# Performance work log

Hardware: AMD Instinct MI355X
Metric: run time of the kernel (lower is better)

## Reference

```python
import jax, jax.numpy as jnp
import numpy as np

N_NODES = 50000
N_EDGES = 800000
IN_DIM = 64
EDGE_DIM = 16
HID = 128
L = 3
G = 128  # number of graphs in the batch
EPS = 1e-5


def _glorot(key, shape):
    fan_in, fan_out = shape[0], shape[1]
    lim = float(np.sqrt(6.0 / (fan_in + fan_out)))
    return jax.random.uniform(key, shape, jnp.float32, -lim, lim)


def setup_inputs() -> dict:
    key = jax.random.key(0)
    ks = jax.random.split(key, 40)
    inp = {}
    inp["x"] = jax.random.uniform(ks[0], (N_NODES, IN_DIM), jnp.float32)
    inp["edge_index"] = jax.random.randint(ks[1], (2, N_EDGES), 0, N_NODES, jnp.int64)
    inp["edge_attr"] = jax.random.normal(ks[2], (N_EDGES, EDGE_DIM), jnp.float32)
    inp["batch"] = jnp.sort(jax.random.randint(ks[3], (N_NODES,), 0, G, jnp.int64))
    # ligand / protein input MLPs: Linear-ReLU-Linear-ReLU
    inp["lig_w1"] = _glorot(ks[4], (IN_DIM, HID)); inp["lig_b1"] = jnp.zeros((HID,), jnp.float32)
    inp["lig_w2"] = _glorot(ks[5], (HID, HID));    inp["lig_b2"] = jnp.zeros((HID,), jnp.float32)
    inp["prot_w1"] = _glorot(ks[6], (IN_DIM, HID)); inp["prot_b1"] = jnp.zeros((HID,), jnp.float32)
    inp["prot_w2"] = _glorot(ks[7], (HID, HID));    inp["prot_b2"] = jnp.zeros((HID,), jnp.float32)
    # per-layer GINEConv params (stacked over layers)
    inp["edge_w"] = jnp.stack([_glorot(ks[8 + i], (EDGE_DIM, HID)) for i in range(L)])
    inp["edge_b"] = jnp.zeros((L, HID), jnp.float32)
    inp["nn_w1"] = jnp.stack([_glorot(ks[12 + i], (HID, HID)) for i in range(L)])
    inp["nn_b1"] = jnp.zeros((L, HID), jnp.float32)
    inp["nn_w2"] = jnp.stack([_glorot(ks[16 + i], (HID, HID)) for i in range(L)])
    inp["nn_b2"] = jnp.zeros((L, HID), jnp.float32)
    # GraphNorm params: weight=1, bias=0, mean_scale=1
    inp["gn_w"] = jnp.ones((L, HID), jnp.float32)
    inp["gn_b"] = jnp.zeros((L, HID), jnp.float32)
    inp["gn_ms"] = jnp.ones((L, HID), jnp.float32)
    # output head: Linear-ReLU-Linear(1)
    inp["fc_w1"] = _glorot(ks[20], (HID, HID)); inp["fc_b1"] = jnp.zeros((HID,), jnp.float32)
    inp["fc_w2"] = _glorot(ks[21], (HID, 1));   inp["fc_b2"] = jnp.zeros((1,), jnp.float32)
    return inp


def reference(x, edge_index, edge_attr, batch,
              lig_w1, lig_b1, lig_w2, lig_b2,
              prot_w1, prot_b1, prot_w2, prot_b2,
              edge_w, edge_b, nn_w1, nn_b1, nn_w2, nn_b2,
              gn_w, gn_b, gn_ms,
              fc_w1, fc_b1, fc_w2, fc_b2):
    relu = lambda a: jnp.maximum(a, 0)
    src, dst = edge_index[0], edge_index[1]

    # input encoders, merged per node by protein flag (last feature column)
    is_prot = x[:, -1] > 0.5
    h_lig = relu(relu(x @ lig_w1 + lig_b1) @ lig_w2 + lig_b2)
    h_prot = relu(relu(x @ prot_w1 + prot_b1) @ prot_w2 + prot_b2)
    h = jnp.where(is_prot[:, None], h_prot, h_lig)

    # per-graph node counts for GraphNorm
    cnt = jax.ops.segment_sum(jnp.ones((x.shape[0],), jnp.float32), batch, num_segments=G)
    cnt = jnp.maximum(cnt, 1.0)[:, None]

    for l in range(L):
        # GINEConv (eps=0): out = nn(x + sum_{j->i} relu(x_j + lin(e_ji)))
        e = edge_attr @ edge_w[l] + edge_b[l]              # [E, HID]
        msg = relu(h[src] + e)                             # gather + add + relu
        aggr = jax.ops.segment_sum(msg, dst, num_segments=h.shape[0])
        h = aggr + h
        h = relu(h @ nn_w1[l] + nn_b1[l]) @ nn_w2[l] + nn_b2[l]
        # GraphNorm: per-graph mean/var with learnable mean_scale
        mean = jax.ops.segment_sum(h, batch, num_segments=G) / cnt
        hc = h - mean[batch] * gn_ms[l]
        var = jax.ops.segment_sum(hc * hc, batch, num_segments=G) / cnt
        h = gn_w[l] * hc * jax.lax.rsqrt(var[batch] + EPS) + gn_b[l]
        h = relu(h)  # (dropout=0.0 -> identity)

    g = jax.ops.segment_sum(h, batch, num_segments=G)      # global_add_pool
    out = relu(g @ fc_w1 + fc_b1) @ fc_w2 + fc_b2
    return out.reshape(-1)
```

## Files before the change

kernel.cpp:

```cpp
#include <hip/hip_runtime.h>

#define N_NODES 50000
#define N_EDGES 800000
#define IN_DIM  64
#define EDGE_DIM 16
#define HID     128
#define NLAYERS 3
#define NGRAPH  128
#define EPS     1e-5f

typedef __attribute__((ext_vector_type(8))) short bf8_t;
typedef __attribute__((ext_vector_type(4))) short bf4_t;
typedef __attribute__((ext_vector_type(4))) float f32x4;

__device__ __forceinline__ unsigned short f2bf(float x) {
    unsigned u = __float_as_uint(x);
    unsigned r = u + 0x7fffu + ((u >> 16) & 1u);
    return (unsigned short)(r >> 16);
}
__device__ __forceinline__ float bf2f(unsigned short v) {
    return __uint_as_float(((unsigned)v) << 16);
}

__global__ void k_init(int* __restrict__ row_cnt, float* __restrict__ pool,
                       float* __restrict__ gsum, float* __restrict__ gsq) {
    int i = blockIdx.x * blockDim.x + threadIdx.x;
    if (i < N_NODES) row_cnt[i] = 0;
    if (i < NGRAPH * HID) { pool[i] = 0.0f; gsum[i] = 0.0f; gsq[i] = 0.0f; }
}

__global__ __launch_bounds__(NGRAPH) void k_count(const int* __restrict__ batch,
                                                  float* __restrict__ cnt) {
    int g = threadIdx.x;
    int lo = 0, hi = N_NODES;
    while (lo < hi) { int mid = (lo + hi) >> 1; if (batch[mid] < g) lo = mid + 1; else hi = mid; }
    int a = lo;
    lo = 0; hi = N_NODES;
    while (lo < hi) { int mid = (lo + hi) >> 1; if (batch[mid] < g + 1) lo = mid + 1; else hi = mid; }
    cnt[g] = (float)(lo - a);
}

__global__ void k_wconv(const float* __restrict__ nw1, const float* __restrict__ nw2,
                        unsigned short* __restrict__ wt) {
    int idx = blockIdx.x * 256 + threadIdx.x;
    if (idx >= NLAYERS * 2 * HID * HID) return;
    int k = idx & 127;
    int n = (idx >> 7) & 127;
    int which = (idx >> 14) & 1;
    int l = idx >> 15;
    const float* w = (which == 0 ? nw1 : nw2) + l * HID * HID;
    wt[idx] = f2bf(w[k * HID + n]);
}

__global__ void k_wconv_enc(const float* __restrict__ lw1, const float* __restrict__ pw1,
                            const float* __restrict__ lw2, const float* __restrict__ pw2,
                            unsigned short* __restrict__ we) {
    int idx = blockIdx.x * 256 + threadIdx.x;
    if (idx >= 49152) return;
    float v;
    if (idx < 8192)       { int n = idx >> 6, k = idx & 63;            v = lw1[k * HID + n]; }
    else if (idx < 16384) { int r = idx - 8192;  int n = r >> 6, k = r & 63;  v = pw1[k * HID + n]; }
    else if (idx < 32768) { int r = idx - 16384; int n = r >> 7, k = r & 127; v = lw2[k * HID + n]; }
    else                  { int r = idx - 32768; int n = r >> 7, k = r & 127; v = pw2[k * HID + n]; }
    we[idx] = f2bf(v);
}

__global__ void k_wconv_e(const float* __restrict__ ew, const float* __restrict__ eb,
                          unsigned short* __restrict__ wte) {
    int idx = blockIdx.x * 256 + threadIdx.x;
    if (idx >= NLAYERS * 8 * 64 * 8) return;
    int j = idx & 7;
    int lane = (idx >> 3) & 63;
    int t = (idx >> 9) & 7;
    int l = idx >> 12;
    int k = (lane >> 4) * 8 + j;
    int feat = t * 16 + (lane & 15);
    float v = 0.0f;
    if (k < EDGE_DIM)       v = ew[l * EDGE_DIM * HID + k * HID + feat];
    else if (k == EDGE_DIM) v = eb[l * HID + feat];
    wte[idx] = f2bf(v);
}

__global__ void k_hist(const int* __restrict__ dsts, int* __restrict__ row_cnt) {
    int e = blockIdx.x * blockDim.x + threadIdx.x;
    if (e < N_EDGES) atomicAdd(&row_cnt[dsts[e]], 1);
}

__global__ __launch_bounds__(256) void k_scan1(const int* __restrict__ row_cnt,
                                               int* __restrict__ partial) {
    __shared__ int s[256];
    int t = threadIdx.x, b = blockIdx.x;
    int i0 = b * 512 + t;
    int v = 0;
    if (i0 < N_NODES) v += row_cnt[i0];
    if (i0 + 256 < N_NODES) v += row_cnt[i0 + 256];
    s[t] = v; __syncthreads();
    for (int off = 128; off > 0; off >>= 1) {
        if (t < off) s[t] += s[t + off];
        __syncthreads();
    }
    if (t == 0) partial[b] = s[0];
}

#define NCHUNK 98
__global__ __launch_bounds__(128) void k_scan2(int* __restrict__ partial) {
    __shared__ int s[128];
    int t = threadIdx.x;
    int v = (t < NCHUNK) ? partial[t] : 0;
    s[t] = v; __syncthreads();
    for (int off = 1; off < 128; off <<= 1) {
        int x = (t >= off) ? s[t - off] : 0;
        __syncthreads();
        s[t] += x;
        __syncthreads();
    }
    partial[t] = s[t] - v;
}

__global__ __launch_bounds__(512) void k_scan3(const int* __restrict__ row_cnt,
                                               const int* __restrict__ partial,
                                               int* __restrict__ row_start,
                                               int* __restrict__ row_fill) {
    __shared__ int s[512];
    int t = threadIdx.x, b = blockIdx.x;
    int i = b * 512 + t;
    int v = (i < N_NODES) ? row_cnt[i] : 0;
    s[t] = v; __syncthreads();
    for (int off = 1; off < 512; off <<= 1) {
        int x = (t >= off) ? s[t - off] : 0;
        __syncthreads();
        s[t] += x;
        __syncthreads();
    }
    int excl = s[t] - v + partial[b];
    if (i < N_NODES) { row_start[i] = excl; row_fill[i] = excl; }
}

__global__ void k_fill(const int* __restrict__ srcs, const int* __restrict__ dsts,
                       int* __restrict__ row_fill, int2* __restrict__ csr_se) {
    int e = blockIdx.x * blockDim.x + threadIdx.x;
    if (e < N_EDGES) {
        int p = atomicAdd(&row_fill[dsts[e]], 1);
        csr_se[p] = make_int2(srcs[e], e);
    }
}

__global__ __launch_bounds__(256) void k_reorder(const int2* __restrict__ csr_se,
                                                 const float* __restrict__ ea,
                                                 int* __restrict__ csr_src,
                                                 unsigned short* __restrict__ cea) {
    int p = blockIdx.x * blockDim.x + threadIdx.x;
    if (p < N_EDGES) {
        int2 se = csr_se[p];
        csr_src[p] = se.x;
        const float* s = ea + (size_t)se.y * EDGE_DIM;
        float4 a0 = *(const float4*)(s);
        float4 a1 = *(const float4*)(s + 4);
        float4 a2 = *(const float4*)(s + 8);
        float4 a3 = *(const float4*)(s + 12);
        bf8_t v0, v1;
        v0[0] = (short)f2bf(a0.x); v0[1] = (short)f2bf(a0.y);
        v0[2] = (short)f2bf(a0.z); v0[3] = (short)f2bf(a0.w);
        v0[4] = (short)f2bf(a1.x); v0[5] = (short)f2bf(a1.y);
        v0[6] = (short)f2bf(a1.z); v0[7] = (short)f2bf(a1.w);
        v1[0] = (short)f2bf(a2.x); v1[1] = (short)f2bf(a2.y);
        v1[2] = (short)f2bf(a2.z); v1[3] = (short)f2bf(a2.w);
        v1[4] = (short)f2bf(a3.x); v1[5] = (short)f2bf(a3.y);
        v1[6] = (short)f2bf(a3.z); v1[7] = (short)f2bf(a3.w);
        *(bf8_t*)(cea + (size_t)p * EDGE_DIM) = v0;
        *(bf8_t*)(cea + (size_t)p * EDGE_DIM + 8) = v1;
    }
}

#define HS 136
__global__ __launch_bounds__(256, 8) void k_encoder_mfma(
    const float* __restrict__ x,
    const unsigned short* __restrict__ we,
    const float* __restrict__ lb1, const float* __restrict__ lb2,
    const float* __restrict__ pb1, const float* __restrict__ pb2,
    unsigned short* __restrict__ Hbp) {
    __shared__ short h1s[4][16 * HS];
    int w = threadIdx.x >> 6, lane = threadIdx.x & 63;
    int m = lane & 15, quad = lane >> 4;
    int tile = w >> 1, role = w & 1;
    int nb = blockIdx.x * 32 + tile * 16;
    short* hl = h1s[w];
    int nclamp = nb + m; if (nclamp >= N_NODES) nclamp = N_NODES - 1;
    const float* xp = x + (size_t)nclamp * IN_DIM;
    const float* b1 = role ? pb1 : lb1;
    const float* b2 = role ? pb2 : lb2;
    const unsigned short* w1 = we + role * 8192;
    const unsigned short* w2 = we + 16384 + role * 16384;

    f32x4 a1[8];
    #pragma unroll
    for (int t = 0; t < 8; ++t) {
        float bv = b1[t * 16 + m];
        a1[t] = (f32x4){bv, bv, bv, bv};
    }
    #pragma unroll
    for (int s_ = 0; s_ < 2; ++s_) {
        int k0 = s_ * 32 + quad * 8;
        float4 a0 = *(const float4*)(xp + k0);
        float4 a1v = *(const float4*)(xp + k0 + 4);
        bf8_t af;
        af[0] = (short)f2bf(a0.x); af[1] = (short)f2bf(a0.y);
        af[2] = (short)f2bf(a0.z); af[3] = (short)f2bf(a0.w);
        af[4] = (short)f2bf(a1v.x); af[5] = (short)f2bf(a1v.y);
        af[6] = (short)f2bf(a1v.z); af[7] = (short)f2bf(a1v.w);
        #pragma unroll
        for (int t = 0; t < 8; ++t) {
            bf8_t bw = *(const bf8_t*)(w1 + (t * 16 + m) * 64 + k0);
            a1[t] = __builtin_amdgcn_mfma_f32_16x16x32_bf16(af, bw, a1[t], 0, 0, 0);
        }
    }
    #pragma unroll
    for (int t = 0; t < 8; ++t)
        #pragma unroll
        for (int r = 0; r < 4; ++r)
            hl[(quad * 4 + r) * HS + t * 16 + m] = (short)f2bf(fmaxf(a1[t][r], 0.0f));
    __syncthreads();
    f32x4 a2[8];
    #pragma unroll
    for (int t = 0; t < 8; ++t) {
        float bv = b2[t * 16 + m];
        a2[t] = (f32x4){bv, bv, bv, bv};
    }
    #pragma unroll
    for (int s_ = 0; s_ < 4; ++s_) {
        int k0 = s_ * 32 + quad * 8;
        bf8_t af = *(const bf8_t*)(hl + m * HS + k0);
        #pragma unroll
        for (int t = 0; t < 8; ++t) {
            bf8_t bw = *(const bf8_t*)(w2 + (t * 16 + m) * 128 + k0);
            a2[t] = __builtin_amdgcn_mfma_f32_16x16x32_bf16(af, bw, a2[t], 0, 0, 0);
        }
    }
    #pragma unroll
    for (int r = 0; r < 4; ++r) {
        int node = nb + quad * 4 + r;
        if (node < N_NODES) {
            bool prot = x[(size_t)node * IN_DIM + (IN_DIM - 1)] > 0.5f;
            if (prot == (role == 1)) {
                bf8_t o;
                #pragma unroll
                for (int t = 0; t < 8; ++t)
                    o[t] = (short)f2bf(fmaxf(a2[t][r], 0.0f));
                *(bf8_t*)(Hbp + (size_t)node * HID + m * 8) = o;
            }
        }
    }
}

__global__ __launch_bounds__(256, 8) void k_gather(
    const int* __restrict__ csr_src, const unsigned short* __restrict__ cea,
    const int* __restrict__ row_start, const int* __restrict__ row_end,
    const unsigned short* __restrict__ wte,
    const unsigned short* __restrict__ Hbp, unsigned short* __restrict__ Abp) {
    int w = threadIdx.x >> 6, lane = threadIdx.x & 63;
    int m = lane & 15, quad = lane >> 4;
    int n = blockIdx.x * 2 + (w >> 1);
    int half = w & 1;

    bf8_t bw[4];
    #pragma unroll
    for (int t = 0; t < 4; ++t)
        bw[t] = *(const bf8_t*)(wte + ((size_t)(half * 4 + t) * 64 + lane) * 8);

    float acc[4];
    #pragma unroll
    for (int t = 0; t < 4; ++t) acc[t] = 0.0f;

    int p  = __builtin_amdgcn_readfirstlane(row_start[n]);
    int pe = __builtin_amdgcn_readfirstlane(row_end[n]);

    const f32x4 zc = (f32x4){0.0f, 0.0f, 0.0f, 0.0f};

    for (; p + 16 <= pe; p += 16) {
        bf8_t af = (bf8_t){0, 0, 0, 0, 0, 0, 0, 0};
        if (quad < 2)
            af = *(const bf8_t*)(cea + (size_t)(p + m) * EDGE_DIM + quad * 8);
        else if (quad == 2)
            af[0] = (short)0x3F80;
        int sr[4];
        #pragma unroll
        for (int r = 0; r < 4; ++r) sr[r] = csr_src[p + quad * 4 + r];
        bf4_t hrow[4];
        #pragma unroll
        for (int r = 0; r < 4; ++r)
            hrow[r] = *(const bf4_t*)(Hbp + (size_t)sr[r] * HID + m * 8 + half * 4);
        f32x4 d[4];
        #pragma unroll
        for (int t = 0; t < 4; ++t)
            d[t] = __builtin_amdgcn_mfma_f32_16x16x32_bf16(af, bw[t], zc, 0, 0, 0);
        #pragma unroll
        for (int t = 0; t < 4; ++t)
            #pragma unroll
            for (int r = 0; r < 4; ++r)
                acc[t] += fmaxf(bf2f((unsigned short)hrow[r][t]) + d[t][r], 0.0f);
    }
    int rem = pe - p;
    if (rem > 0) {
        bf8_t af = (bf8_t){0, 0, 0, 0, 0, 0, 0, 0};
        if (quad < 2 && m < rem)
            af = *(const bf8_t*)(cea + (size_t)(p + m) * EDGE_DIM + quad * 8);
        else if (quad == 2)
            af[0] = (short)0x3F80;
        int sr[4];
        #pragma unroll
        for (int r = 0; r < 4; ++r) {
            int idx = p + quad * 4 + r; if (idx >= pe) idx = pe - 1;
            sr[r] = csr_src[idx];
        }
        bf4_t hrow[4];
        #pragma unroll
        for (int r = 0; r < 4; ++r)
            hrow[r] = *(const bf4_t*)(Hbp + (size_t)sr[r] * HID + m * 8 + half * 4);
        f32x4 d[4];
        #pragma unroll
        for (int t = 0; t < 4; ++t)
            d[t] = __builtin_amdgcn_mfma_f32_16x16x32_bf16(af, bw[t], zc, 0, 0, 0);
        #pragma unroll
        for (int t = 0; t < 4; ++t)
            #pragma unroll
            for (int r = 0; r < 4; ++r)
                if (quad * 4 + r < rem)
                    acc[t] += fmaxf(bf2f((unsigned short)hrow[r][t]) + d[t][r], 0.0f);
    }
    #pragma unroll
    for (int t = 0; t < 4; ++t) {
        acc[t] += __shfl_xor(acc[t], 16);
        acc[t] += __shfl_xor(acc[t], 32);
    }
    float asel = (quad == 0) ? acc[0] : (quad == 1) ? acc[1] : (quad == 2) ? acc[2] : acc[3];
    float self_ = bf2f(Hbp[(size_t)n * HID + m * 8 + half * 4 + quad]);
    Abp[(size_t)n * HID + (half * 4 + quad) * 16 + m] = f2bf(asel + self_);
}

#define MLP_NODES_PER_BLOCK 64
__global__ __launch_bounds__(256) void k_mlp_mfma(
    const unsigned short* __restrict__ Abp, const int* __restrict__ batch,
    const unsigned short* __restrict__ wt1, const unsigned short* __restrict__ wt2,
    const float* __restrict__ b1, const float* __restrict__ b2,
    unsigned short* __restrict__ Hb, float* __restrict__ gsum, float* __restrict__ gsq) {
    __shared__ short h1s[4 * 16 * HS];
    int w = threadIdx.x >> 6;
    int lane = threadIdx.x & 63;
    int m = lane & 15;
    int quad = lane >> 4;
    int nb = blockIdx.x * MLP_NODES_PER_BLOCK + w * 16;
    short* hw = h1s + w * 16 * HS;

    int nclamp = nb + m; if (nclamp >= N_NODES) nclamp = N_NODES - 1;
    const unsigned short* Ap = Abp + (size_t)nclamp * HID;
    f32x4 acc1[8];
    #pragma unroll
    for (int t = 0; t < 8; ++t) {
        float bv = b1[t * 16 + m];
        acc1[t] = (f32x4){bv, bv, bv, bv};
    }
    #pragma unroll
    for (int s_ = 0; s_ < 4; ++s_) {
        int k0 = s_ * 32 + quad * 8;
        bf8_t af = *(const bf8_t*)(Ap + k0);
        #pragma unroll
        for (int t = 0; t < 8; ++t) {
            bf8_t bf = *(const bf8_t*)(wt1 + (t * 16 + m) * HID + k0);
            acc1[t] = __builtin_amdgcn_mfma_f32_16x16x32_bf16(af, bf, acc1[t], 0, 0, 0);
        }
    }
    #pragma unroll
    for (int t = 0; t < 8; ++t)
        #pragma unroll
        for (int r = 0; r < 4; ++r) {
            float v = fmaxf(acc1[t][r], 0.0f);
            hw[(quad * 4 + r) * HS + t * 16 + m] = (short)f2bf(v);
        }
    __syncthreads();
    f32x4 acc2[8];
    #pragma unroll
    for (int t = 0; t < 8; ++t) {
        float bv = b2[t * 16 + m];
        acc2[t] = (f32x4){bv, bv, bv, bv};
    }
    #pragma unroll
    for (int s_ = 0; s_ < 4; ++s_) {
        int k0 = s_ * 32 + quad * 8;
        bf8_t af = *(const bf8_t*)(hw + m * HS + k0);
        #pragma unroll
        for (int t = 0; t < 8; ++t) {
            bf8_t bf = *(const bf8_t*)(wt2 + (t * 16 + m) * HID + k0);
            acc2[t] = __builtin_amdgcn_mfma_f32_16x16x32_bf16(af, bf, acc2[t], 0, 0, 0);
        }
    }
    #pragma unroll
    for (int t = 0; t < 8; ++t)
        #pragma unroll
        for (int r = 0; r < 4; ++r) {
            int node = nb + quad * 4 + r;
            if (node < N_NODES) Hb[(size_t)node * HID + t * 16 + m] = f2bf(acc2[t][r]);
        }
    int blast = nb + 15 < N_NODES ? batch[nb + 15] : -1;
    int g0 = batch[nb < N_NODES ? nb : N_NODES - 1];
    if (nb + 15 < N_NODES && g0 == blast) {
        #pragma unroll
        for (int t = 0; t < 8; ++t) {
            float s = 0.0f, q = 0.0f;
            #pragma unroll
            for (int r = 0; r < 4; ++r) { float v = acc2[t][r]; s += v; q += v * v; }
            s += __shfl_xor(s, 16); q += __shfl_xor(q, 16);
            s += __shfl_xor(s, 32); q += __shfl_xor(q, 32);
            if (quad == 0) {
                atomicAdd(&gsum[g0 * HID + t * 16 + m], s);
                atomicAdd(&gsq[g0 * HID + t * 16 + m], q);
            }
        }
    } else {
        #pragma unroll
        for (int t = 0; t < 8; ++t)
            #pragma unroll
            for (int r = 0; r < 4; ++r) {
                int node = nb + quad * 4 + r;
                if (node < N_NODES) {
                    int g = batch[node];
                    float v = acc2[t][r];
                    atomicAdd(&gsum[g * HID + t * 16 + m], v);
                    atomicAdd(&gsq[g * HID + t * 16 + m], v * v);
                }
            }
    }
}

__global__ __launch_bounds__(HID) void k_stats(
    float* __restrict__ gsum, float* __restrict__ gsq,
    const float* __restrict__ cnt,
    const float* __restrict__ gw, const float* __restrict__ gb,
    const float* __restrict__ gms,
    float* __restrict__ sc, float* __restrict__ of) {
    int g = blockIdx.x;
    int t = threadIdx.x;
    float c = fmaxf(cnt[g], 1.0f);
    float mean = gsum[g * HID + t] / c;
    float msq  = gsq[g * HID + t] / c;
    float ms = gms[t];
    float var = msq - mean * mean * ms * (2.0f - ms);
    var = fmaxf(var, 0.0f);
    float istd = rsqrtf(var + EPS);
    float s = gw[t] * istd;
    sc[g * HID + t] = s;
    of[g * HID + t] = gb[t] - s * mean * ms;
    gsum[g * HID + t] = 0.0f;
    gsq[g * HID + t]  = 0.0f;
}

#define NORM_N 8
__global__ __launch_bounds__(HID) void k_norm(
    const unsigned short* __restrict__ Hb, const int* __restrict__ batch,
    const float* __restrict__ sc, const float* __restrict__ of,
    unsigned short* __restrict__ Hbp, float* __restrict__ pool, int accumulate) {
    int n0 = blockIdx.x * NORM_N;
    int t = threadIdx.x;
    int m = t & 15, tt = t >> 4;
    int g0 = batch[n0], gN = batch[n0 + NORM_N - 1];
    if (g0 == gN) {
        float ssc = sc[g0 * HID + t], sof = of[g0 * HID + t];
        float ps = 0.0f;
        #pragma unroll
        for (int i = 0; i < NORM_N; ++i) {
            float v = fmaxf(bf2f(Hb[(size_t)(n0 + i) * HID + t]) * ssc + sof, 0.0f);
            Hbp[(size_t)(n0 + i) * HID + m * 8 + tt] = f2bf(v);
            ps += v;
        }
        if (accumulate) atomicAdd(&pool[g0 * HID + t], ps);
    } else {
        #pragma unroll
        for (int i = 0; i < NORM_N; ++i) {
            int g = batch[n0 + i];
            float v = fmaxf(bf2f(Hb[(size_t)(n0 + i) * HID + t]) * sc[g * HID + t] + of[g * HID + t], 0.0f);
            Hbp[(size_t)(n0 + i) * HID + m * 8 + tt] = f2bf(v);
            if (accumulate) atomicAdd(&pool[g * HID + t], v);
        }
    }
}

__global__ __launch_bounds__(HID) void k_head(
    const float* __restrict__ pool,
    const float* __restrict__ fw1, const float* __restrict__ fb1,
    const float* __restrict__ fw2, const float* __restrict__ fb2,
    float* __restrict__ out) {
    __shared__ float ps[HID];
    __shared__ float red[2];
    int g = blockIdx.x;
    int t = threadIdx.x;
    ps[t] = pool[g * HID + t];
    __syncthreads();
    float acc = fb1[t];
    #pragma unroll 4
    for (int k = 0; k < HID; ++k) acc = fmaf(ps[k], fw1[k * HID + t], acc);
    float p = fmaxf(acc, 0.0f) * fw2[t];
    #pragma unroll
    for (int off = 32; off > 0; off >>= 1) p += __shfl_down(p, off, 64);
    if ((t & 63) == 0) red[t >> 6] = p;
    __syncthreads();
    if (t == 0) out[g] = red[0] + red[1] + fb2[0];
}

extern "C" void kernel_launch(void* const* d_in, const int* in_sizes, int n_in,
                              void* d_out, int out_size, void* d_ws, size_t ws_size,
                              hipStream_t stream) {
    const float* x     = (const float*)d_in[0];
    const int*   ei    = (const int*)d_in[1];
    const float* ea    = (const float*)d_in[2];
    const int*   batch = (const int*)d_in[3];
    const float* lw1 = (const float*)d_in[4];
    const float* lb1 = (const float*)d_in[5];
    const float* lw2 = (const float*)d_in[6];
    const float* lb2 = (const float*)d_in[7];
    const float* pw1 = (const float*)d_in[8];
    const float* pb1 = (const float*)d_in[9];
    const float* pw2 = (const float*)d_in[10];
    const float* pb2 = (const float*)d_in[11];
    const float* ew  = (const float*)d_in[12];
    const float* eb  = (const float*)d_in[13];
    const float* nw1 = (const float*)d_in[14];
    const float* nb1 = (const float*)d_in[15];
    const float* nw2 = (const float*)d_in[16];
    const float* nb2 = (const float*)d_in[17];
    const float* gw  = (const float*)d_in[18];
    const float* gb  = (const float*)d_in[19];
    const float* gms = (const float*)d_in[20];
    const float* fw1 = (const float*)d_in[21];
    const float* fb1 = (const float*)d_in[22];
    const float* fw2 = (const float*)d_in[23];
    const float* fb2 = (const float*)d_in[24];
    float* out = (float*)d_out;

    float* ws   = (float*)d_ws;
    float* H    = ws;
    float* A    = H    + (size_t)N_NODES * HID;
    float* gsum = A    + (size_t)N_NODES * HID;
    float* gsq  = gsum + NGRAPH * HID;
    float* sc   = gsq  + NGRAPH * HID;
    float* of   = sc   + NGRAPH * HID;
    float* pool = of   + NGRAPH * HID;
    float* cnt  = pool + NGRAPH * HID;
    int* row_cnt   = (int*)(cnt + NGRAPH);
    int* row_start = row_cnt + N_NODES;
    int* row_fill  = row_start + N_NODES;
    int* partial   = row_fill + N_NODES;
    int* csr_src   = partial + 128;
    unsigned short* cea  = (unsigned short*)(csr_src + N_EDGES);
    unsigned short* wt   = cea + (size_t)N_EDGES * EDGE_DIM;
    unsigned short* wenc = wt + NLAYERS * 2 * HID * HID;
    unsigned short* wte  = wenc + 49152;
    unsigned short* Hbp  = wte + NLAYERS * 8 * 64 * 8;
    unsigned short* Hb   = (unsigned short*)H;
    unsigned short* Abp  = (unsigned short*)A;
    int2* csr_se = (int2*)(Abp + (size_t)N_NODES * HID);

    const int* srcs = ei;
    const int* dsts = ei + N_EDGES;

    k_init<<<(N_NODES + 255) / 256, 256, 0, stream>>>(row_cnt, pool, gsum, gsq);
    k_count<<<1, NGRAPH, 0, stream>>>(batch, cnt);
    k_wconv<<<(NLAYERS * 2 * HID * HID + 255) / 256, 256, 0, stream>>>(nw1, nw2, wt);
    k_wconv_enc<<<(49152 + 255) / 256, 256, 0, stream>>>(lw1, pw1, lw2, pw2, wenc);
    k_wconv_e<<<(NLAYERS * 8 * 64 * 8 + 255) / 256, 256, 0, stream>>>(ew, eb, wte);
    k_hist<<<(N_EDGES + 255) / 256, 256, 0, stream>>>(dsts, row_cnt);
    k_scan1<<<NCHUNK, 256, 0, stream>>>(row_cnt, partial);
    k_scan2<<<1, 128, 0, stream>>>(partial);
    k_scan3<<<NCHUNK, 512, 0, stream>>>(row_cnt, partial, row_start, row_fill);
    k_fill<<<(N_EDGES + 255) / 256, 256, 0, stream>>>(srcs, dsts, row_fill, csr_se);
    k_reorder<<<(N_EDGES + 255) / 256, 256, 0, stream>>>(csr_se, ea, csr_src, cea);

    k_encoder_mfma<<<(N_NODES + 31) / 32, 256, 0, stream>>>(
        x, wenc, lb1, lb2, pb1, pb2, Hbp);

    int mlp_blocks = (N_NODES + MLP_NODES_PER_BLOCK - 1) / MLP_NODES_PER_BLOCK;
    for (int l = 0; l < NLAYERS; ++l) {
        k_gather<<<N_NODES / 2, 256, 0, stream>>>(
            csr_src, cea, row_start, row_fill,
            wte + (size_t)l * 4096, Hbp, Abp);
        k_mlp_mfma<<<mlp_blocks, 256, 0, stream>>>(
            Abp, batch,
            wt + (size_t)l * 2 * HID * HID,
            wt + (size_t)l * 2 * HID * HID + HID * HID,
            nb1 + l * HID, nb2 + l * HID, Hb, gsum, gsq);
        k_stats<<<NGRAPH, HID, 0, stream>>>(gsum, gsq, cnt,
                                            gw + l * HID, gb + l * HID, gms + l * HID,
                                            sc, of);
        k_norm<<<N_NODES / NORM_N, HID, 0, stream>>>(
            Hb, batch, sc, of, Hbp, pool, (l == NLAYERS - 1) ? 1 : 0);
    }
    k_head<<<NGRAPH, HID, 0, stream>>>(pool, fw1, fb1, fw2, fb2, out);
}
```

Baseline: 674.1 us.

## Split MLP output features across wave pairs to cut accumulator registers

Each 16-node tile in the fused node MLP is now handled by two waves, each computing half of the 128 output features, and a block covers 32 nodes instead of 64. Per-wave accumulator arrays shrink from 8 to 4 MFMA tiles, and launch bounds ask for 6 blocks per SM, so more waves can be resident to hide the latency of weight and activation loads. The cost is that each input row is loaded by two waves, the grid has twice as many blocks, and the statistics atomics are spread over more waves.

```diff
diff --git a/kernel.cpp b/kernel.cpp
--- a/kernel.cpp
+++ b/kernel.cpp
@@ -337,26 +337,28 @@
     Abp[(size_t)n * HID + (half * 4 + quad) * 16 + m] = f2bf(asel + self_);
 }
 
-#define MLP_NODES_PER_BLOCK 64
-__global__ __launch_bounds__(256) void k_mlp_mfma(
+#define MLP_NODES_PER_BLOCK 32
+__global__ __launch_bounds__(256, 6) void k_mlp_mfma(
     const unsigned short* __restrict__ Abp, const int* __restrict__ batch,
     const unsigned short* __restrict__ wt1, const unsigned short* __restrict__ wt2,
     const float* __restrict__ b1, const float* __restrict__ b2,
     unsigned short* __restrict__ Hb, float* __restrict__ gsum, float* __restrict__ gsq) {
-    __shared__ short h1s[4 * 16 * HS];
+    __shared__ short h1s[2][16 * HS];
     int w = threadIdx.x >> 6;
     int lane = threadIdx.x & 63;
     int m = lane & 15;
     int quad = lane >> 4;
-    int nb = blockIdx.x * MLP_NODES_PER_BLOCK + w * 16;
-    short* hw = h1s + w * 16 * HS;
+    int tile = w >> 1, role = w & 1;
+    int nb = blockIdx.x * MLP_NODES_PER_BLOCK + tile * 16;
+    short* hw = h1s[tile];
+    int fbase = role * 64;
 
     int nclamp = nb + m; if (nclamp >= N_NODES) nclamp = N_NODES - 1;
     const unsigned short* Ap = Abp + (size_t)nclamp * HID;
-    f32x4 acc1[8];
-    #pragma unroll
-    for (int t = 0; t < 8; ++t) {
-        float bv = b1[t * 16 + m];
+    f32x4 acc1[4];
+    #pragma unroll
+    for (int t = 0; t < 4; ++t) {
+        float bv = b1[fbase + t * 16 + m];
         acc1[t] = (f32x4){bv, bv, bv, bv};
     }
     #pragma unroll
@@ -364,23 +366,23 @@
         int k0 = s_ * 32 + quad * 8;
         bf8_t af = *(const bf8_t*)(Ap + k0);
         #pragma unroll
-        for (int t = 0; t < 8; ++t) {
-            bf8_t bf = *(const bf8_t*)(wt1 + (t * 16 + m) * HID + k0);
+        for (int t = 0; t < 4; ++t) {
+            bf8_t bf = *(const bf8_t*)(wt1 + (size_t)(fbase + t * 16 + m) * HID + k0);
             acc1[t] = __builtin_amdgcn_mfma_f32_16x16x32_bf16(af, bf, acc1[t], 0, 0, 0);
         }
     }
     #pragma unroll
-    for (int t = 0; t < 8; ++t)
+    for (int t = 0; t < 4; ++t)
         #pragma unroll
         for (int r = 0; r < 4; ++r) {
             float v = fmaxf(acc1[t][r], 0.0f);
-            hw[(quad * 4 + r) * HS + t * 16 + m] = (short)f2bf(v);
+            hw[(quad * 4 + r) * HS + fbase + t * 16 + m] = (short)f2bf(v);
         }
     __syncthreads();
-    f32x4 acc2[8];
-    #pragma unroll
-    for (int t = 0; t < 8; ++t) {
-        float bv = b2[t * 16 + m];
+    f32x4 acc2[4];
+    #pragma unroll
+    for (int t = 0; t < 4; ++t) {
+        float bv = b2[fbase + t * 16 + m];
         acc2[t] = (f32x4){bv, bv, bv, bv};
     }
     #pragma unroll
@@ -388,44 +390,44 @@
         int k0 = s_ * 32 + quad * 8;
         bf8_t af = *(const bf8_t*)(hw + m * HS + k0);
         #pragma unroll
-        for (int t = 0; t < 8; ++t) {
-            bf8_t bf = *(const bf8_t*)(wt2 + (t * 16 + m) * HID + k0);
+        for (int t = 0; t < 4; ++t) {
+            bf8_t bf = *(const bf8_t*)(wt2 + (size_t)(fbase + t * 16 + m) * HID + k0);
             acc2[t] = __builtin_amdgcn_mfma_f32_16x16x32_bf16(af, bf, acc2[t], 0, 0, 0);
         }
     }
     #pragma unroll
-    for (int t = 0; t < 8; ++t)
+    for (int t = 0; t < 4; ++t)
         #pragma unroll
         for (int r = 0; r < 4; ++r) {
             int node = nb + quad * 4 + r;
-            if (node < N_NODES) Hb[(size_t)node * HID + t * 16 + m] = f2bf(acc2[t][r]);
+            if (node < N_NODES) Hb[(size_t)node * HID + fbase + t * 16 + m] = f2bf(acc2[t][r]);
         }
     int blast = nb + 15 < N_NODES ? batch[nb + 15] : -1;
     int g0 = batch[nb < N_NODES ? nb : N_NODES - 1];
     if (nb + 15 < N_NODES && g0 == blast) {
         #pragma unroll
-        for (int t = 0; t < 8; ++t) {
+        for (int t = 0; t < 4; ++t) {
             float s = 0.0f, q = 0.0f;
             #pragma unroll
             for (int r = 0; r < 4; ++r) { float v = acc2[t][r]; s += v; q += v * v; }
             s += __shfl_xor(s, 16); q += __shfl_xor(q, 16);
             s += __shfl_xor(s, 32); q += __shfl_xor(q, 32);
             if (quad == 0) {
-                atomicAdd(&gsum[g0 * HID + t * 16 + m], s);
-                atomicAdd(&gsq[g0 * HID + t * 16 + m], q);
+                atomicAdd(&gsum[g0 * HID + fbase + t * 16 + m], s);
+                atomicAdd(&gsq[g0 * HID + fbase + t * 16 + m], q);
             }
         }
     } else {
         #pragma unroll
-        for (int t = 0; t < 8; ++t)
+        for (int t = 0; t < 4; ++t)
             #pragma unroll
             for (int r = 0; r < 4; ++r) {
                 int node = nb + quad * 4 + r;
                 if (node < N_NODES) {
                     int g = batch[node];
                     float v = acc2[t][r];
-                    atomicAdd(&gsum[g * HID + t * 16 + m], v);
-                    atomicAdd(&gsq[g * HID + t * 16 + m], v * v);
+                    atomicAdd(&gsum[g * HID + fbase + t * 16 + m], v);
+                    atomicAdd(&gsq[g * HID + fbase + t * 16 + m], v * v);
                 }
             }
     }
```

New measurement: 659.2 us. -2.2%, faster.
